# Optimization experiments

Measured on AMD Instinct MI355X. Metric: run time of the kernel, lower is better.

## Reference

```python
import jax, jax.numpy as jnp
import numpy as np

V, E, F, C, H, L = 12000, 512, 2048, 128, 1024, 49

def setup_inputs() -> dict:
    key = jax.random.key(0)
    ks = jax.random.split(key, 20)
    s = 0.02
    return {
        "captions": jax.random.randint(ks[0], (64, 32), 0, V),
        "features": jax.random.normal(ks[1], (64, L, F), jnp.float32),
        "category_enc": jax.random.normal(ks[2], (64, C), jnp.float32),
        "emb": jax.random.uniform(ks[3], (V, E), jnp.float32, -0.1, 0.1),
        "W_ih": jax.random.normal(ks[4], (4 * H, E + F + C), jnp.float32) * s,
        "b_ih": jnp.zeros((4 * H,), jnp.float32),
        "W_hh": jax.random.normal(ks[5], (4 * H, H), jnp.float32) * s,
        "b_hh": jnp.zeros((4 * H,), jnp.float32),
        "fc_W": jax.random.uniform(ks[6], (V, H), jnp.float32, -0.1, 0.1),
        "fc_b": jnp.zeros((V,), jnp.float32),
        "Wh0": jax.random.normal(ks[7], (H, F), jnp.float32) * s,
        "bh0": jnp.zeros((H,), jnp.float32),
        "Wc0": jax.random.normal(ks[8], (H, F), jnp.float32) * s,
        "bc0": jnp.zeros((H,), jnp.float32),
        "att_W": jax.random.normal(ks[9], (F, H), jnp.float32) * s,
        "att_U": jax.random.normal(ks[10], (H, H), jnp.float32) * s,
        "att_v": jax.random.normal(ks[11], (H,), jnp.float32) * s,
    }

def reference(captions, features, category_enc, emb, W_ih, b_ih, W_hh, b_hh,
              fc_W, fc_b, Wh0, bh0, Wc0, bc0, att_W, att_U, att_v):
    # init hidden/cell from mean-pooled features
    mean_feat = features.mean(axis=1)                      # [B, F]
    h = mean_feat @ Wh0.T + bh0                            # [B, H]
    c = mean_feat @ Wc0.T + bc0                            # [B, H]
    feat_proj = jnp.einsum('blf,fa->bla', features, att_W)  # [B, L, H] precompute
    embed = emb[captions]                                  # [B, T, E]

    def step(carry, x_t):
        h, c = carry
        # Bahdanau additive attention
        e = jnp.tanh(feat_proj + (h @ att_U)[:, None, :])  # [B, L, H]
        score = e @ att_v                                  # [B, L]
        w = jax.nn.softmax(score, axis=-1)                 # [B, L]
        context = jnp.einsum('bl,blf->bf', w, features)    # [B, F]
        x = jnp.concatenate([x_t, context, category_enc], axis=1)
        gates = x @ W_ih.T + b_ih + h @ W_hh.T + b_hh      # [B, 4H]
        i, f, g, o = jnp.split(gates, 4, axis=1)
        c2 = jax.nn.sigmoid(f) * c + jax.nn.sigmoid(i) * jnp.tanh(g)
        h2 = jax.nn.sigmoid(o) * jnp.tanh(c2)              # dropout is identity in eval
        out = h2 @ fc_W.T + fc_b                           # [B, V]
        return (h2, c2), (out, w)

    (_, _), (outs, ws) = jax.lax.scan(step, (h, c), jnp.swapaxes(embed, 0, 1))
    return jnp.swapaxes(outs, 0, 1), jnp.swapaxes(ws, 0, 1)
```

## Files before the change

### kernel.cpp

```cpp
#include <hip/hip_runtime.h>
#include <hip/hip_bf16.h>

#define BB 64
#define TT 32
#define VV 12000
#define EE 512
#define FF 2048
#define CDIM 128
#define HH 1024
#define LL 49
#define XKLEN 2688
#define XGLEN 640

typedef __attribute__((ext_vector_type(8))) short bf16x8;
typedef __attribute__((ext_vector_type(4))) float f32x4;

__device__ __forceinline__ unsigned short bf16_rn(float x) {
  unsigned u = __float_as_uint(x);
  u += 0x7FFFu + ((u >> 16) & 1u);
  return (unsigned short)(u >> 16);
}
__device__ __forceinline__ float bf16_tof(unsigned short h) {
  return __uint_as_float(((unsigned)h) << 16);
}
__device__ __forceinline__ void split2(float x, short& hi, short& lo) {
  unsigned short h = bf16_rn(x);
  float r = x - bf16_tof(h);
  hi = (short)h;
  lo = (short)bf16_rn(r);
}
__device__ __forceinline__ bf16x8 cvt8(const float* f) {
  bf16x8 o;
#pragma unroll
  for (int e = 0; e < 8; ++e) o[e] = (short)bf16_rn(f[e]);
  return o;
}
__device__ __forceinline__ void gload16(const void* g, void* l) {
  __builtin_amdgcn_global_load_lds(
      (const __attribute__((address_space(1))) void*)g,
      (__attribute__((address_space(3))) void*)l, 16, 0, 0);
}

__global__ __launch_bounds__(256) void step1_k(
    const short* __restrict__ hHi, const short* __restrict__ hLi,
    const short* __restrict__ attUt,
    const short* __restrict__ featpB,
    const float* __restrict__ att_v,
    const short* __restrict__ Whb,
    float* __restrict__ partS,
    float* __restrict__ ghh)
{
  __shared__ float red4[4][64][5];
  __shared__ float hu_s[16][17];
  __shared__ float av_s[16];
  __shared__ float red3[3][64][17];
  const int tid = threadIdx.x;
  const int w = tid >> 6, lane = tid & 63;
  const int r = lane & 15, kg = lane >> 4;

  if (blockIdx.x < 256) {
    const int bid = blockIdx.x;
    const int id = (bid & 7) * 32 + (bid >> 3);
    const int nt = id >> 2, mh = id & 3;
    const int kb = w * 256;

    if (tid < 16) av_s[tid] = att_v[nt * 16 + tid];

    const short* wp = attUt + (size_t)(nt * 16 + r) * HH + kb + kg * 8;
    const short* ap = hHi + (size_t)(mh * 16 + r) * HH + kb + kg * 8;
    f32x4 acc = {};
#pragma unroll
    for (int k0 = 0; k0 < 256; k0 += 32) {
      bf16x8 bf = *(const bf16x8*)(wp + k0);
      bf16x8 af = *(const bf16x8*)(ap + k0);
      acc = __builtin_amdgcn_mfma_f32_16x16x32_bf16(af, bf, acc, 0, 0, 0);
    }
#pragma unroll
    for (int q = 0; q < 4; ++q)
      red4[w][lane][q] = acc[q];
    __syncthreads();

    {
      const int bl = tid >> 4, a = tid & 15;
      const int sl = (bl >> 2) * 16 + a;
      const int ii = bl & 3;
      hu_s[bl][a] = red4[0][sl][ii] + red4[1][sl][ii]
                  + red4[2][sl][ii] + red4[3][sl][ii];
    }
    __syncthreads();

    for (int task = tid; task < 16 * LL; task += 256) {
      const int bl = task / LL, l = task - bl * LL;
      const int b = mh * 16 + bl;
      const short* fp = featpB + ((size_t)nt * 3136 + (size_t)b * LL + l) * 16;
      bf16x8 v0 = *(const bf16x8*)&fp[0];
      bf16x8 v1 = *(const bf16x8*)&fp[8];
      float s = 0.f;
#pragma unroll
      for (int a = 0; a < 8; ++a)
        s += tanhf(bf16_tof((unsigned short)v0[a]) + hu_s[bl][a]) * av_s[a];
#pragma unroll
      for (int a = 0; a < 8; ++a)
        s += tanhf(bf16_tof((unsigned short)v1[a]) + hu_s[bl][8 + a]) * av_s[8 + a];
      partS[(size_t)nt * 3136 + (size_t)mh * 784 + task] = s;
    }
  } else {
    const int bid = blockIdx.x - 256;
    const int id = (bid & 7) * 32 + (bid >> 3);
    const int nt = id >> 2, mq = id & 3;
    const int brow = mq * 16 + r;
    f32x4 acc0 = {}, acc1 = {}, acc2 = {}, acc3 = {};
#pragma unroll
    for (int c = 0; c < 8; ++c) {
      const int hk = (w * 8 + c) * 32;
      const short* a_h = hHi + (size_t)brow * HH + hk + kg * 8;
      const short* a_l = hLi + (size_t)brow * HH + hk + kg * 8;
      const short* w0p = Whb + (size_t)(0 * 1024 + nt * 16 + r) * HH + hk + kg * 8;
      const short* w1p = Whb + (size_t)(1 * 1024 + nt * 16 + r) * HH + hk + kg * 8;
      const short* w2p = Whb + (size_t)(2 * 1024 + nt * 16 + r) * HH + hk + kg * 8;
      const short* w3p = Whb + (size_t)(3 * 1024 + nt * 16 + r) * HH + hk + kg * 8;
      bf16x8 af  = *(const bf16x8*)a_h;
      bf16x8 alf = *(const bf16x8*)a_l;
      bf16x8 b0 = *(const bf16x8*)w0p;
      acc0 = __builtin_amdgcn_mfma_f32_16x16x32_bf16(af,  b0, acc0, 0, 0, 0);
      acc0 = __builtin_amdgcn_mfma_f32_16x16x32_bf16(alf, b0, acc0, 0, 0, 0);
      bf16x8 b1 = *(const bf16x8*)w1p;
      acc1 = __builtin_amdgcn_mfma_f32_16x16x32_bf16(af,  b1, acc1, 0, 0, 0);
      acc1 = __builtin_amdgcn_mfma_f32_16x16x32_bf16(alf, b1, acc1, 0, 0, 0);
      bf16x8 b2 = *(const bf16x8*)w2p;
      acc2 = __builtin_amdgcn_mfma_f32_16x16x32_bf16(af,  b2, acc2, 0, 0, 0);
      acc2 = __builtin_amdgcn_mfma_f32_16x16x32_bf16(alf, b2, acc2, 0, 0, 0);
      bf16x8 b3 = *(const bf16x8*)w3p;
      acc3 = __builtin_amdgcn_mfma_f32_16x16x32_bf16(af,  b3, acc3, 0, 0, 0);
      acc3 = __builtin_amdgcn_mfma_f32_16x16x32_bf16(alf, b3, acc3, 0, 0, 0);
    }
    if (w != 0) {
#pragma unroll
      for (int q = 0; q < 4; ++q) {
        red3[w - 1][lane][0 * 4 + q] = acc0[q];
        red3[w - 1][lane][1 * 4 + q] = acc1[q];
        red3[w - 1][lane][2 * 4 + q] = acc2[q];
        red3[w - 1][lane][3 * 4 + q] = acc3[q];
      }
    }
    __syncthreads();
    if (w == 0) {
      const int j = nt * 16 + r;
#pragma unroll
      for (int q = 0; q < 4; ++q) {
        const int b = mq * 16 + kg * 4 + q;
        float g0 = acc0[q], g1 = acc1[q], g2 = acc2[q], g3 = acc3[q];
#pragma unroll
        for (int p = 0; p < 3; ++p) {
          g0 += red3[p][lane][0 * 4 + q];
          g1 += red3[p][lane][1 * 4 + q];
          g2 += red3[p][lane][2 * 4 + q];
          g3 += red3[p][lane][3 * 4 + q];
        }
        float* gh = ghh + (size_t)b * 4096;
        gh[0 * 1024 + j] = g0;
        gh[1 * 1024 + j] = g1;
        gh[2 * 1024 + j] = g2;
        gh[3 * 1024 + j] = g3;
      }
    }
  }
}

__global__ __launch_bounds__(256) void step2_k(
    const short* __restrict__ featCtx,
    const float* __restrict__ partS,
    const float* __restrict__ ghh,
    const float* __restrict__ gxg,
    float* __restrict__ cbuf,
    short* __restrict__ hHo, short* __restrict__ hLo,
    float* __restrict__ w_out, int t)
{
  __shared__ float sw[16][52];
  __shared__ float ctx_p[2][16][72];
  const int tid = threadIdx.x;
  const int w = tid >> 6, lane = tid & 63;
  const int bid = blockIdx.x;
  const int id = (bid & 7) * 32 + (bid >> 3);
  const int nt = id >> 2, mq = id & 3;

  for (int idx = tid; idx < 16 * LL; idx += 256) {
    const float* ps = partS + (size_t)mq * 784 + idx;
    float s = 0.f;
#pragma unroll 8
    for (int a = 0; a < 64; ++a) s += ps[(size_t)a * 3136];
    sw[idx / LL][idx % LL] = s;
  }
  __syncthreads();
#pragma unroll
  for (int i = 0; i < 4; ++i) {
    const int bl = w * 4 + i;
    float v = (lane < LL) ? sw[bl][lane] : -1e30f;
    float m = v;
#pragma unroll
    for (int off = 32; off > 0; off >>= 1) m = fmaxf(m, __shfl_xor(m, off));
    float e = (lane < LL) ? expf(v - m) : 0.f;
    float s = e;
#pragma unroll
    for (int off = 32; off > 0; off >>= 1) s += __shfl_xor(s, off);
    float ww = e / s;
    if (lane < LL) {
      sw[bl][lane] = ww;
      if (nt == 0)
        w_out[((size_t)(mq * 16 + bl) * TT + t) * LL + lane] = ww;
    }
  }
  __syncthreads();

  {
    const int bl = tid >> 4, tsub = tid & 15;
    const int e8 = (tsub & 7) * 8, lpar = tsub >> 3;
    const size_t base =
        ((size_t)nt * 3136 + (size_t)(mq * 16 + bl) * LL) * 64 + e8;
    float s[8] = {};
    for (int l = lpar; l < LL; l += 2) {
      bf16x8 v = *(const bf16x8*)&featCtx[base + (size_t)l * 64];
      const float wl = sw[bl][l];
#pragma unroll
      for (int e = 0; e < 8; ++e)
        s[e] += wl * bf16_tof((unsigned short)v[e]);
    }
#pragma unroll
    for (int e = 0; e < 8; ++e)
      ctx_p[lpar][bl][e8 + e] = s[e];
  }
  __syncthreads();

  {
    const int bl = tid >> 4, jr = tid & 15;
    const int b = mq * 16 + bl;
    const int j = nt * 16 + jr;
    const float* gh = ghh + (size_t)b * 4096;
    const float* gx = gxg + ((size_t)t * 64 + b) * 4096;
    float gi = gh[0 * 1024 + j] + gx[0 * 1024 + j]
             + ctx_p[0][bl][0 * 16 + jr] + ctx_p[1][bl][0 * 16 + jr];
    float gf = gh[1 * 1024 + j] + gx[1 * 1024 + j]
             + ctx_p[0][bl][1 * 16 + jr] + ctx_p[1][bl][1 * 16 + jr];
    float gg = gh[2 * 1024 + j] + gx[2 * 1024 + j]
             + ctx_p[0][bl][2 * 16 + jr] + ctx_p[1][bl][2 * 16 + jr];
    float go = gh[3 * 1024 + j] + gx[3 * 1024 + j]
             + ctx_p[0][bl][3 * 16 + jr] + ctx_p[1][bl][3 * 16 + jr];
    float si = 1.f / (1.f + expf(-gi));
    float sf = 1.f / (1.f + expf(-gf));
    float so = 1.f / (1.f + expf(-go));
    const size_t ci = (size_t)b * HH + j;
    float cc = sf * cbuf[ci] + si * tanhf(gg);
    float hh = so * tanhf(cc);
    cbuf[ci] = cc;
    short hi, lo; split2(hh, hi, lo);
    hHo[ci] = hi;
    hLo[ci] = lo;
  }
}

__global__ __launch_bounds__(256) void tgemm2_k(
    const short* __restrict__ A,
    const short* __restrict__ attWt,
    const short* __restrict__ Wctxb,
    short* __restrict__ featpB, short* __restrict__ featCtx)
{
  __shared__ short lA[128 * 32];
  __shared__ short lW[128 * 32];
  const int tid = threadIdx.x;
  const int w = tid >> 6, lane = tid & 63;
  const int r = lane & 15, kg = lane >> 4;
  const int M = BB * LL, K = FF;
  const bool ctx = (blockIdx.y >= 8);
  const short* Wb = ctx ? Wctxb : attWt;
  const int n0 = (ctx ? (blockIdx.y - 8) : blockIdx.y) * 128;
  const int m0 = blockIdx.x * 128;
  const int srow = tid >> 2, scol = (tid & 3) * 8;

  f32x4 acc[2][8] = {};
  for (int k0 = 0; k0 < K; k0 += 32) {
    __syncthreads();
#pragma unroll
    for (int j = 0; j < 2; ++j) {
      const int row = j * 64 + srow;
      int ar = m0 + row; if (ar >= M) ar = M - 1;
      const size_t lbase = (size_t)j * 4096 + (size_t)w * 1024;
      gload16(&A[(size_t)ar * K + k0 + scol], (char*)lA + lbase);
      gload16(&Wb[(size_t)(n0 + row) * K + k0 + scol], (char*)lW + lbase);
    }
    __syncthreads();
    bf16x8 a0 = *(const bf16x8*)&lA[(w * 32 +  0 + r) * 32 + kg * 8];
    bf16x8 a1 = *(const bf16x8*)&lA[(w * 32 + 16 + r) * 32 + kg * 8];
#pragma unroll
    for (int nf = 0; nf < 8; ++nf) {
      bf16x8 wf = *(const bf16x8*)&lW[(nf * 16 + r) * 32 + kg * 8];
      acc[0][nf] = __builtin_amdgcn_mfma_f32_16x16x32_bf16(a0, wf, acc[0][nf], 0, 0, 0);
      acc[1][nf] = __builtin_amdgcn_mfma_f32_16x16x32_bf16(a1, wf, acc[1][nf], 0, 0, 0);
    }
  }
#pragma unroll
  for (int nf = 0; nf < 8; ++nf) {
    const int col = n0 + nf * 16 + r;
#pragma unroll
    for (int mf = 0; mf < 2; ++mf)
#pragma unroll
      for (int q = 0; q < 4; ++q) {
        const int grow = m0 + w * 32 + mf * 16 + kg * 4 + q;
        if (grow < M) {
          const short v = (short)bf16_rn(acc[mf][nf][q]);
          if (!ctx) {
            const int ntc = col >> 4, aa = col & 15;
            featpB[((size_t)ntc * 3136 + grow) * 16 + aa] = v;
          } else {
            const int gate = col >> 10, ntc = (col >> 4) & 63, jj = col & 15;
            featCtx[((size_t)ntc * 3136 + grow) * 64 + gate * 16 + jj] = v;
          }
        }
      }
  }
}

__global__ __launch_bounds__(256) void tgemm3_k(
    const short* __restrict__ Ah, const short* __restrict__ Al,
    const short* __restrict__ Wb, const float* __restrict__ bias,
    float* __restrict__ outs)
{
  __shared__ short lAh[128 * 32];
  __shared__ short lAl[128 * 32];
  __shared__ short lW [128 * 32];
  const int tid = threadIdx.x;
  const int w = tid >> 6, lane = tid & 63;
  const int r = lane & 15, kg = lane >> 4;
  const int m0 = blockIdx.x * 128;
  const int n0 = blockIdx.y * 128;
  const int srow = tid >> 2, scol = (tid & 3) * 8;

  f32x4 acc[2][8] = {};
  for (int k0 = 0; k0 < XGLEN; k0 += 32) {
    __syncthreads();
#pragma unroll
    for (int j = 0; j < 2; ++j) {
      const int row = j * 64 + srow;
      const size_t lbase = (size_t)j * 4096 + (size_t)w * 1024;
      gload16(&Ah[(size_t)(m0 + row) * XGLEN + k0 + scol], (char*)lAh + lbase);
      gload16(&Al[(size_t)(m0 + row) * XGLEN + k0 + scol], (char*)lAl + lbase);
      gload16(&Wb[(size_t)(n0 + row) * XGLEN + k0 + scol], (char*)lW + lbase);
    }
    __syncthreads();
    bf16x8 ah0 = *(const bf16x8*)&lAh[(w * 32 +  0 + r) * 32 + kg * 8];
    bf16x8 ah1 = *(const bf16x8*)&lAh[(w * 32 + 16 + r) * 32 + kg * 8];
    bf16x8 al0 = *(const bf16x8*)&lAl[(w * 32 +  0 + r) * 32 + kg * 8];
    bf16x8 al1 = *(const bf16x8*)&lAl[(w * 32 + 16 + r) * 32 + kg * 8];
#pragma unroll
    for (int nf = 0; nf < 8; ++nf) {
      bf16x8 wf = *(const bf16x8*)&lW[(nf * 16 + r) * 32 + kg * 8];
      acc[0][nf] = __builtin_amdgcn_mfma_f32_16x16x32_bf16(ah0, wf, acc[0][nf], 0, 0, 0);
      acc[0][nf] = __builtin_amdgcn_mfma_f32_16x16x32_bf16(al0, wf, acc[0][nf], 0, 0, 0);
      acc[1][nf] = __builtin_amdgcn_mfma_f32_16x16x32_bf16(ah1, wf, acc[1][nf], 0, 0, 0);
      acc[1][nf] = __builtin_amdgcn_mfma_f32_16x16x32_bf16(al1, wf, acc[1][nf], 0, 0, 0);
    }
  }
#pragma unroll
  for (int nf = 0; nf < 8; ++nf) {
    const int colv = n0 + nf * 16 + r;
    const float bv = bias[colv];
#pragma unroll
    for (int mf = 0; mf < 2; ++mf)
#pragma unroll
      for (int q = 0; q < 4; ++q) {
        const int grow = m0 + w * 32 + mf * 16 + kg * 4 + q;
        outs[(size_t)grow * 4096 + colv] = acc[mf][nf][q] + bv;
      }
  }
}

__global__ __launch_bounds__(256) void bgemm_k(
    const short* __restrict__ Ah, const short* __restrict__ Al,
    const short* __restrict__ Wb, const float* __restrict__ bias,
    float* __restrict__ outs)
{
  __shared__ short lAh[128 * 32];
  __shared__ short lAl[128 * 32];
  __shared__ short lW [128 * 32];
  const int tid = threadIdx.x;
  const int w = tid >> 6, lane = tid & 63;
  const int r = lane & 15, kg = lane >> 4;
  const int m0 = blockIdx.x * 128;
  const int n0 = blockIdx.y * 128;
  const int srow = tid >> 2, scol = (tid & 3) * 8;

  f32x4 acc[2][8] = {};
  for (int k0 = 0; k0 < HH; k0 += 32) {
    __syncthreads();
#pragma unroll
    for (int j = 0; j < 2; ++j) {
      const int row = j * 64 + srow;
      int wr = n0 + row; if (wr >= VV) wr = VV - 1;
      const size_t lbase = (size_t)j * 4096 + (size_t)w * 1024;
      gload16(&Ah[(size_t)(m0 + row) * HH + k0 + scol], (char*)lAh + lbase);
      gload16(&Al[(size_t)(m0 + row) * HH + k0 + scol], (char*)lAl + lbase);
      gload16(&Wb[(size_t)wr * HH + k0 + scol], (char*)lW + lbase);
    }
    __syncthreads();
    bf16x8 ah0 = *(const bf16x8*)&lAh[(w * 32 +  0 + r) * 32 + kg * 8];
    bf16x8 ah1 = *(const bf16x8*)&lAh[(w * 32 + 16 + r) * 32 + kg * 8];
    bf16x8 al0 = *(const bf16x8*)&lAl[(w * 32 +  0 + r) * 32 + kg * 8];
    bf16x8 al1 = *(const bf16x8*)&lAl[(w * 32 + 16 + r) * 32 + kg * 8];
#pragma unroll
    for (int nf = 0; nf < 8; ++nf) {
      bf16x8 wf = *(const bf16x8*)&lW[(nf * 16 + r) * 32 + kg * 8];
      acc[0][nf] = __builtin_amdgcn_mfma_f32_16x16x32_bf16(ah0, wf, acc[0][nf], 0, 0, 0);
      acc[0][nf] = __builtin_amdgcn_mfma_f32_16x16x32_bf16(al0, wf, acc[0][nf], 0, 0, 0);
      acc[1][nf] = __builtin_amdgcn_mfma_f32_16x16x32_bf16(ah1, wf, acc[1][nf], 0, 0, 0);
      acc[1][nf] = __builtin_amdgcn_mfma_f32_16x16x32_bf16(al1, wf, acc[1][nf], 0, 0, 0);
    }
  }
#pragma unroll
  for (int nf = 0; nf < 8; ++nf) {
    const int colv = n0 + nf * 16 + r;
    if (colv < VV) {
      const float bv = bias[colv];
#pragma unroll
      for (int mf = 0; mf < 2; ++mf)
#pragma unroll
        for (int q = 0; q < 4; ++q) {
          const int grow = m0 + w * 32 + mf * 16 + kg * 4 + q;
          const int tt = grow >> 6, b = grow & 63;
          outs[((size_t)b * TT + tt) * VV + colv] = acc[mf][nf][q] + bv;
        }
    }
  }
}

__global__ __launch_bounds__(256) void h0c0_k(
    const short* __restrict__ mfb,
    const short* __restrict__ Wh0b, const float* __restrict__ bh0,
    const short* __restrict__ Wc0b, const float* __restrict__ bc0,
    short* __restrict__ h0H, short* __restrict__ h0L,
    float* __restrict__ cbuf)
{
  const int tid = threadIdx.x;
  const int w = tid >> 6, l = tid & 63;
  const int r = l & 15, kg = l >> 4;
  const bool cpath = blockIdx.x >= 32;
  const int nb = blockIdx.x & 31;
  const short* Wb = cpath ? Wc0b : Wh0b;
  const float* bias = cpath ? bc0 : bh0;
  const int nslice = w >> 1, mbase = (w & 1) * 2;
  const int n0 = nb * 32 + nslice * 16;
  const int nrow = n0 + r;
  const short* wp = Wb + (size_t)nrow * FF + kg * 8;
  const short* ap = mfb + (size_t)(mbase * 16 + r) * FF + kg * 8;
  f32x4 acc[2] = {};
  for (int k0 = 0; k0 < FF; k0 += 32) {
    bf16x8 bf = *(const bf16x8*)(wp + k0);
#pragma unroll
    for (int m = 0; m < 2; ++m) {
      bf16x8 af = *(const bf16x8*)(ap + (size_t)(16 * m) * FF + k0);
      acc[m] = __builtin_amdgcn_mfma_f32_16x16x32_bf16(af, bf, acc[m], 0, 0, 0);
    }
  }
  const float bv = bias[nrow];
#pragma unroll
  for (int m = 0; m < 2; ++m)
#pragma unroll
    for (int q = 0; q < 4; ++q) {
      const int mm = (mbase + m) * 16 + kg * 4 + q;
      const float v = acc[m][q] + bv;
      if (cpath) {
        cbuf[(size_t)mm * HH + nrow] = v;
      } else {
        short hi, lo; split2(v, hi, lo);
        h0H[(size_t)mm * HH + nrow] = hi;
        h0L[(size_t)mm * HH + nrow] = lo;
      }
    }
}

__global__ __launch_bounds__(256) void transpose2_k(
    const float* __restrict__ attU, short* __restrict__ attUt,
    const float* __restrict__ attW, short* __restrict__ attWt)
{
  __shared__ float tile[32][33];
  const bool isW = blockIdx.y >= 32;
  const float* in = isW ? attW : attU;
  short* out = isW ? attWt : attUt;
  const int R = isW ? FF : HH;
  const int br = (isW ? (blockIdx.y - 32) : blockIdx.y) * 32;
  const int bc = blockIdx.x * 32;
  int tx = threadIdx.x & 31, ty4 = (threadIdx.x >> 5) << 2;
#pragma unroll
  for (int i = 0; i < 4; ++i)
    tile[ty4 + i][tx] = in[(size_t)(br + ty4 + i) * HH + bc + tx];
  __syncthreads();
#pragma unroll
  for (int i = 0; i < 4; ++i)
    out[(size_t)(bc + ty4 + i) * R + br + tx] = (short)bf16_rn(tile[tx][ty4 + i]);
}

#define S_FEATB   6422528ULL
#define C1  (S_FEATB)
#define C2  (C1 + 12288000ULL)
#define C3  (C2 + 4194304ULL)
#define C4  (C3 + 2097152ULL)
#define C5  (C4 + 2097152ULL)
#define C6  (C5 + 2621440ULL)
#define C7  (C6 + 8388608ULL)
#define C8  (C7 + 1310720ULL)
#define C9  (C8 + 4096ULL)
#define C10 (C9 + 131072ULL)

__global__ __launch_bounds__(256) void prep_k(
    const float* __restrict__ features, const float* __restrict__ fc_W,
    const float* __restrict__ W_hh, const float* __restrict__ Wh0,
    const float* __restrict__ Wc0, const float* __restrict__ W_ih,
    const int* __restrict__ captions, const float* __restrict__ emb,
    const float* __restrict__ cat,
    const float* __restrict__ b_ih, const float* __restrict__ b_hh,
    short* __restrict__ featb, short* __restrict__ fcWb,
    short* __restrict__ Whb, short* __restrict__ Wh0b,
    short* __restrict__ Wc0b, short* __restrict__ Wxg,
    short* __restrict__ Wctxb, short* __restrict__ xgH,
    short* __restrict__ xgL, float* __restrict__ bg,
    short* __restrict__ mfb)
{
  const size_t stride = (size_t)gridDim.x * 256;
  for (size_t ii = (size_t)blockIdx.x * 256 + threadIdx.x; ii < (C10 >> 3);
       ii += stride) {
    const size_t i = ii << 3;
    float f[8];
    if (i < C1) {
      *(float4*)&f[0] = *(const float4*)&features[i];
      *(float4*)&f[4] = *(const float4*)&features[i + 4];
      *(bf16x8*)&featb[i] = cvt8(f);
    } else if (i < C2) {
      const size_t j = i - C1;
      *(float4*)&f[0] = *(const float4*)&fc_W[j];
      *(float4*)&f[4] = *(const float4*)&fc_W[j + 4];
      *(bf16x8*)&fcWb[j] = cvt8(f);
    } else if (i < C3) {
      const size_t j = i - C2;
      *(float4*)&f[0] = *(const float4*)&W_hh[j];
      *(float4*)&f[4] = *(const float4*)&W_hh[j + 4];
      *(bf16x8*)&Whb[j] = cvt8(f);
    } else if (i < C4) {
      const size_t j = i - C3;
      *(float4*)&f[0] = *(const float4*)&Wh0[j];
      *(float4*)&f[4] = *(const float4*)&Wh0[j + 4];
      *(bf16x8*)&Wh0b[j] = cvt8(f);
    } else if (i < C5) {
      const size_t j = i - C4;
      *(float4*)&f[0] = *(const float4*)&Wc0[j];
      *(float4*)&f[4] = *(const float4*)&Wc0[j + 4];
      *(bf16x8*)&Wc0b[j] = cvt8(f);
    } else if (i < C6) {
      const size_t j = i - C5;
      const int n = (int)(j / XGLEN), k = (int)(j % XGLEN);
      const int ks = (k < EE) ? k : (EE + FF + (k - EE));
      const float* src = &W_ih[(size_t)n * XKLEN + ks];
      *(float4*)&f[0] = *(const float4*)&src[0];
      *(float4*)&f[4] = *(const float4*)&src[4];
      *(bf16x8*)&Wxg[j] = cvt8(f);
    } else if (i < C7) {
      const size_t j = i - C6;
      const int n = (int)(j / FF), k = (int)(j % FF);
      const float* src = &W_ih[(size_t)n * XKLEN + EE + k];
      *(float4*)&f[0] = *(const float4*)&src[0];
      *(float4*)&f[4] = *(const float4*)&src[4];
      *(bf16x8*)&Wctxb[j] = cvt8(f);
    } else if (i < C8) {
      const size_t j = i - C7;
      const int row = (int)(j / XGLEN), k = (int)(j % XGLEN);
      const int t = row >> 6, b = row & 63;
      const float* src;
      if (k < EE) {
        const int cap = captions[b * TT + t];
        src = &emb[(size_t)cap * EE + k];
      } else {
        src = &cat[(size_t)b * CDIM + (k - EE)];
      }
      *(float4*)&f[0] = *(const float4*)&src[0];
      *(float4*)&f[4] = *(const float4*)&src[4];
      bf16x8 hi8, lo8;
#pragma unroll
      for (int e = 0; e < 8; ++e) {
        short h, l2; split2(f[e], h, l2);
        hi8[e] = h; lo8[e] = l2;
      }
      *(bf16x8*)&xgH[j] = hi8;
      *(bf16x8*)&xgL[j] = lo8;
    } else if (i < C9) {
      const size_t j = i - C8;
      float4 a0 = *(const float4*)&b_ih[j];
      float4 a1 = *(const float4*)&b_ih[j + 4];
      float4 c0 = *(const float4*)&b_hh[j];
      float4 c1 = *(const float4*)&b_hh[j + 4];
      float4 o0 = make_float4(a0.x + c0.x, a0.y + c0.y, a0.z + c0.z, a0.w + c0.w);
      float4 o1 = make_float4(a1.x + c1.x, a1.y + c1.y, a1.z + c1.z, a1.w + c1.w);
      *(float4*)&bg[j] = o0;
      *(float4*)&bg[j + 4] = o1;
    } else {
      const size_t j = i - C9;
      const int b = (int)(j >> 11), f0 = (int)(j & 2047);
      float s[8] = {};
      for (int l = 0; l < LL; ++l) {
        const float* src = &features[((size_t)b * LL + l) * FF + f0];
        float4 u0 = *(const float4*)&src[0];
        float4 u1 = *(const float4*)&src[4];
        s[0] += u0.x; s[1] += u0.y; s[2] += u0.z; s[3] += u0.w;
        s[4] += u1.x; s[5] += u1.y; s[6] += u1.z; s[7] += u1.w;
      }
#pragma unroll
      for (int e = 0; e < 8; ++e) s[e] *= (1.f / 49.f);
      *(bf16x8*)&mfb[j] = cvt8(s);
    }
  }
}

extern "C" void kernel_launch(void* const* d_in, const int* in_sizes, int n_in,
                              void* d_out, int out_size, void* d_ws, size_t ws_size,
                              hipStream_t stream) {
  const int*   captions = (const int*)  d_in[0];
  const float* features = (const float*)d_in[1];
  const float* category = (const float*)d_in[2];
  const float* emb      = (const float*)d_in[3];
  const float* W_ih     = (const float*)d_in[4];
  const float* b_ih     = (const float*)d_in[5];
  const float* W_hh     = (const float*)d_in[6];
  const float* b_hh     = (const float*)d_in[7];
  const float* fc_W     = (const float*)d_in[8];
  const float* fc_b     = (const float*)d_in[9];
  const float* Wh0      = (const float*)d_in[10];
  const float* bh0      = (const float*)d_in[11];
  const float* Wc0      = (const float*)d_in[12];
  const float* bc0      = (const float*)d_in[13];
  const float* att_W    = (const float*)d_in[14];
  const float* att_U    = (const float*)d_in[15];
  const float* att_v    = (const float*)d_in[16];

  float* outs  = (float*)d_out;
  float* w_out = outs + (size_t)BB * TT * VV;

  char* p = (char*)d_ws;
  auto alloc = [&](size_t bytes) {
    char* q = p; p += (bytes + 255) & ~(size_t)255; return q;
  };
  short* attUt  = (short*)alloc((size_t)HH * HH * 2);
  short* attWt  = (short*)alloc((size_t)HH * FF * 2);
  short* featb  = (short*)alloc((size_t)BB * LL * FF * 2);
  short* fcWb   = (short*)alloc((size_t)VV * HH * 2);
  short* Wctxb  = (short*)alloc((size_t)4096 * FF * 2);
  short* Whb    = (short*)alloc((size_t)4096 * HH * 2);
  short* Wxg    = (short*)alloc((size_t)4096 * XGLEN * 2);
  short* Wh0b   = (short*)alloc((size_t)HH * FF * 2);
  short* Wc0b   = (short*)alloc((size_t)HH * FF * 2);
  short* mfb    = (short*)alloc((size_t)BB * FF * 2);
  short* h0H    = (short*)alloc((size_t)BB * HH * 2);
  short* h0L    = (short*)alloc((size_t)BB * HH * 2);
  short* xgH    = (short*)alloc((size_t)2048 * XGLEN * 2);
  short* xgL    = (short*)alloc((size_t)2048 * XGLEN * 2);
  short* featpB = (short*)alloc((size_t)64 * 3136 * 16 * 2);
  short* featCtx= (short*)alloc((size_t)64 * 3136 * 64 * 2);
  float* gxg    = (float*)alloc((size_t)2048 * 4096 * 4);
  float* ghh    = (float*)alloc((size_t)64 * 4096 * 4);
  float* cbuf   = (float*)alloc((size_t)BB * HH * 4);
  float* partS  = (float*)alloc((size_t)64 * 3136 * 4);
  float* bg     = (float*)alloc(4096 * 4);
  short* hallH = featb;
  short* hallL = featb + (size_t)TT * BB * HH;

  prep_k<<<2048, 256, 0, stream>>>(
      features, fc_W, W_hh, Wh0, Wc0, W_ih, captions, emb, category,
      b_ih, b_hh,
      featb, fcWb, Whb, Wh0b, Wc0b, Wxg, Wctxb, xgH, xgL, bg, mfb);
  transpose2_k<<<dim3(32, 96), 256, 0, stream>>>(att_U, attUt, att_W, attWt);
  h0c0_k<<<64, 256, 0, stream>>>(mfb, Wh0b, bh0, Wc0b, bc0, h0H, h0L, cbuf);
  tgemm2_k<<<dim3(25, 40), 256, 0, stream>>>(featb, attWt, Wctxb, featpB, featCtx);
  tgemm3_k<<<dim3(16, 32), 256, 0, stream>>>(xgH, xgL, Wxg, bg, gxg);

  for (int t = 0; t < TT; ++t) {
    const short* hHi = (t == 0) ? h0H : hallH + (size_t)(t - 1) * BB * HH;
    const short* hLi = (t == 0) ? h0L : hallL + (size_t)(t - 1) * BB * HH;
    step1_k<<<512, 256, 0, stream>>>(
        hHi, hLi, attUt, featpB, att_v, Whb, partS, ghh);
    step2_k<<<256, 256, 0, stream>>>(
        featCtx, partS, ghh, gxg, cbuf,
        hallH + (size_t)t * BB * HH, hallL + (size_t)t * BB * HH, w_out, t);
  }

  bgemm_k<<<dim3(16, 94), 256, 0, stream>>>(hallH, hallL, fcWb, fc_b, outs);
}
```

Before: 1.582 ms.

## Split W_hh recurrent GEMM over K into two halves and use fast transcendentals

The recurrent h@W_hh GEMM blocks in step1_k are split along the K dimension into two halves, giving 512 GEMM blocks instead of 256 (768 total). Each half writes partial gate sums to a separate ghh buffer, and step2_k adds the two together. The goal is to fill more CUs on the serial per-timestep critical path, at the cost of extra partial-sum traffic. It also replaces tanhf/expf with __expf-based fast tanh and sigmoid, which lowers transcendental cost but may reduce accuracy.

```diff
diff --git a/kernel.cpp b/kernel.cpp
--- a/kernel.cpp
+++ b/kernel.cpp
@@ -39,6 +39,12 @@
   __builtin_amdgcn_global_load_lds(
       (const __attribute__((address_space(1))) void*)g,
       (__attribute__((address_space(3))) void*)l, 16, 0, 0);
+}
+__device__ __forceinline__ float fast_tanh(float x) {
+  return 1.f - 2.f / (__expf(2.f * x) + 1.f);
+}
+__device__ __forceinline__ float fast_sig(float x) {
+  return 1.f / (1.f + __expf(-x));
 }
 
 __global__ __launch_bounds__(256) void step1_k(
@@ -98,21 +104,24 @@
       float s = 0.f;
 #pragma unroll
       for (int a = 0; a < 8; ++a)
-        s += tanhf(bf16_tof((unsigned short)v0[a]) + hu_s[bl][a]) * av_s[a];
+        s += fast_tanh(bf16_tof((unsigned short)v0[a]) + hu_s[bl][a]) * av_s[a];
 #pragma unroll
       for (int a = 0; a < 8; ++a)
-        s += tanhf(bf16_tof((unsigned short)v1[a]) + hu_s[bl][8 + a]) * av_s[8 + a];
+        s += fast_tanh(bf16_tof((unsigned short)v1[a]) + hu_s[bl][8 + a]) * av_s[8 + a];
       partS[(size_t)nt * 3136 + (size_t)mh * 784 + task] = s;
     }
   } else {
-    const int bid = blockIdx.x - 256;
-    const int id = (bid & 7) * 32 + (bid >> 3);
-    const int nt = id >> 2, mq = id & 3;
+    const int b2 = blockIdx.x - 256;
+    const int id = (b2 & 7) * 64 + (b2 >> 3);
+    const int nt = id >> 3;
+    const int mq = (id >> 1) & 3;
+    const int kq = id & 1;
+    const int ks = kq * 512;
     const int brow = mq * 16 + r;
     f32x4 acc0 = {}, acc1 = {}, acc2 = {}, acc3 = {};
 #pragma unroll
-    for (int c = 0; c < 8; ++c) {
-      const int hk = (w * 8 + c) * 32;
+    for (int c = 0; c < 4; ++c) {
+      const int hk = ks + (w * 4 + c) * 32;
       const short* a_h = hHi + (size_t)brow * HH + hk + kg * 8;
       const short* a_l = hLi + (size_t)brow * HH + hk + kg * 8;
       const short* w0p = Whb + (size_t)(0 * 1024 + nt * 16 + r) * HH + hk + kg * 8;
@@ -127,9 +136,9 @@
       bf16x8 b1 = *(const bf16x8*)w1p;
       acc1 = __builtin_amdgcn_mfma_f32_16x16x32_bf16(af,  b1, acc1, 0, 0, 0);
       acc1 = __builtin_amdgcn_mfma_f32_16x16x32_bf16(alf, b1, acc1, 0, 0, 0);
-      bf16x8 b2 = *(const bf16x8*)w2p;
-      acc2 = __builtin_amdgcn_mfma_f32_16x16x32_bf16(af,  b2, acc2, 0, 0, 0);
-      acc2 = __builtin_amdgcn_mfma_f32_16x16x32_bf16(alf, b2, acc2, 0, 0, 0);
+      bf16x8 b2v = *(const bf16x8*)w2p;
+      acc2 = __builtin_amdgcn_mfma_f32_16x16x32_bf16(af,  b2v, acc2, 0, 0, 0);
+      acc2 = __builtin_amdgcn_mfma_f32_16x16x32_bf16(alf, b2v, acc2, 0, 0, 0);
       bf16x8 b3 = *(const bf16x8*)w3p;
       acc3 = __builtin_amdgcn_mfma_f32_16x16x32_bf16(af,  b3, acc3, 0, 0, 0);
       acc3 = __builtin_amdgcn_mfma_f32_16x16x32_bf16(alf, b3, acc3, 0, 0, 0);
@@ -157,7 +166,7 @@
           g2 += red3[p][lane][2 * 4 + q];
           g3 += red3[p][lane][3 * 4 + q];
         }
-        float* gh = ghh + (size_t)b * 4096;
+        float* gh = ghh + (size_t)kq * 64 * 4096 + (size_t)b * 4096;
         gh[0 * 1024 + j] = g0;
         gh[1 * 1024 + j] = g1;
         gh[2 * 1024 + j] = g2;
@@ -199,7 +208,7 @@
     float m = v;
 #pragma unroll
     for (int off = 32; off > 0; off >>= 1) m = fmaxf(m, __shfl_xor(m, off));
-    float e = (lane < LL) ? expf(v - m) : 0.f;
+    float e = (lane < LL) ? __expf(v - m) : 0.f;
     float s = e;
 #pragma unroll
     for (int off = 32; off > 0; off >>= 1) s += __shfl_xor(s, off);
@@ -235,22 +244,23 @@
     const int bl = tid >> 4, jr = tid & 15;
     const int b = mq * 16 + bl;
     const int j = nt * 16 + jr;
-    const float* gh = ghh + (size_t)b * 4096;
+    const float* gh0 = ghh + (size_t)b * 4096;
+    const float* gh1 = ghh + (size_t)64 * 4096 + (size_t)b * 4096;
     const float* gx = gxg + ((size_t)t * 64 + b) * 4096;
-    float gi = gh[0 * 1024 + j] + gx[0 * 1024 + j]
+    float gi = gh0[0 * 1024 + j] + gh1[0 * 1024 + j] + gx[0 * 1024 + j]
              + ctx_p[0][bl][0 * 16 + jr] + ctx_p[1][bl][0 * 16 + jr];
-    float gf = gh[1 * 1024 + j] + gx[1 * 1024 + j]
+    float gf = gh0[1 * 1024 + j] + gh1[1 * 1024 + j] + gx[1 * 1024 + j]
              + ctx_p[0][bl][1 * 16 + jr] + ctx_p[1][bl][1 * 16 + jr];
-    float gg = gh[2 * 1024 + j] + gx[2 * 1024 + j]
+    float gg = gh0[2 * 1024 + j] + gh1[2 * 1024 + j] + gx[2 * 1024 + j]
              + ctx_p[0][bl][2 * 16 + jr] + ctx_p[1][bl][2 * 16 + jr];
-    float go = gh[3 * 1024 + j] + gx[3 * 1024 + j]
+    float go = gh0[3 * 1024 + j] + gh1[3 * 1024 + j] + gx[3 * 1024 + j]
              + ctx_p[0][bl][3 * 16 + jr] + ctx_p[1][bl][3 * 16 + jr];
-    float si = 1.f / (1.f + expf(-gi));
-    float sf = 1.f / (1.f + expf(-gf));
-    float so = 1.f / (1.f + expf(-go));
+    float si = fast_sig(gi);
+    float sf = fast_sig(gf);
+    float so = fast_sig(go);
     const size_t ci = (size_t)b * HH + j;
-    float cc = sf * cbuf[ci] + si * tanhf(gg);
-    float hh = so * tanhf(cc);
+    float cc = sf * cbuf[ci] + si * fast_tanh(gg);
+    float hh = so * fast_tanh(cc);
     cbuf[ci] = cc;
     short hi, lo; split2(hh, hi, lo);
     hHo[ci] = hi;
@@ -661,7 +671,7 @@
   short* featpB = (short*)alloc((size_t)64 * 3136 * 16 * 2);
   short* featCtx= (short*)alloc((size_t)64 * 3136 * 64 * 2);
   float* gxg    = (float*)alloc((size_t)2048 * 4096 * 4);
-  float* ghh    = (float*)alloc((size_t)64 * 4096 * 4);
+  float* ghh    = (float*)alloc((size_t)2 * 64 * 4096 * 4);
   float* cbuf   = (float*)alloc((size_t)BB * HH * 4);
   float* partS  = (float*)alloc((size_t)64 * 3136 * 4);
   float* bg     = (float*)alloc(4096 * 4);
@@ -680,7 +690,7 @@
   for (int t = 0; t < TT; ++t) {
     const short* hHi = (t == 0) ? h0H : hallH + (size_t)(t - 1) * BB * HH;
     const short* hLi = (t == 0) ? h0L : hallL + (size_t)(t - 1) * BB * HH;
-    step1_k<<<512, 256, 0, stream>>>(
+    step1_k<<<768, 256, 0, stream>>>(
         hHi, hLi, attUt, featpB, att_v, Whb, partS, ghh);
     step2_k<<<256, 256, 0, stream>>>(
         featCtx, partS, ghh, gxg, cbuf,
```

New measurement: 1.473 ms. -6.9%, faster.
